# Kernel tuning notes

Measured on AMD Instinct MI355X. Metric: run time of the kernel, lower is better.

Reference implementation:

```python
import jax, jax.numpy as jnp
import numpy as np

PAD = 32  # integer padding from init_kwargs

def _conv1d_fft(x, weight, bias):
    # x: (B, Cin, L), weight: (Cout, Cin, K), bias: (Cout,)
    B, Cin, L = x.shape
    Cout, _, K = weight.shape
    p = PAD
    padded = (L + 2 * p + 31) & ~31          # round up to multiple of 32
    out_len = 2 * p + L - (K - 1)
    offset = (min(K, L) - 1) // 2 - p
    roll = -((K - 1) // 2) + offset
    # pad kernel to padded length then circularly roll (centers the kernel)
    k_pad = jnp.pad(weight, ((0, 0), (0, 0), (0, padded - K)))
    k_rolled = jnp.roll(k_pad, roll, axis=-1)
    x_fft = jnp.fft.rfft(x, n=padded, axis=-1)          # (B, Cin, F)
    k_fft = jnp.fft.rfft(k_rolled, axis=-1)             # (Cout, Cin, F)
    # multiply-reduce over in_channels == batched complex GEMM over freq bins
    b_fft = jnp.einsum('bif,oif->bof', x_fft, jnp.conj(k_fft))
    # bias enters only the DC bin, scaled by padded length (irfft normalization)
    b_fft = b_fft.at[..., 0].add(bias.astype(b_fft.dtype) * padded)
    b = jnp.fft.irfft(b_fft, n=padded, axis=-1)
    return b[..., :out_len]


def setup_inputs() -> dict:
    key = jax.random.key(0)
    k1, k2, k3 = jax.random.split(key, 3)
    B, Cin, Cout, L, K = 16, 128, 128, 4096, 129
    stdv = 1.0 / np.sqrt(Cin * K)
    x = jax.random.normal(k1, (B, Cin, L), dtype=jnp.float32)
    weight = jax.random.uniform(k2, (Cout, Cin, K), dtype=jnp.float32, minval=-stdv, maxval=stdv)
    bias = jax.random.uniform(k3, (Cout,), dtype=jnp.float32, minval=-stdv, maxval=stdv)
    return {"x": x, "weight": weight, "bias": bias}


def reference(x, weight, bias):
    return _conv1d_fft(x, weight, bias)
```

## Files before the change

### kernel.cpp

```cpp
#include <hip/hip_runtime.h>


typedef _Float16 f16;
typedef _Float16 f16x8 __attribute__((ext_vector_type(8)));
typedef float f32x4 __attribute__((ext_vector_type(4)));

#define NB   16
#define CI   128
#define CO   128
#define LIN  4096
#define KW   129
#define TOUT 4032
#define UPAD 4224
#define KCH  516
#define XT_BYTES ((size_t)NB * UPAD * CI * 2)

__device__ __forceinline__ void gld16(void* lds, const void* g) {
    __builtin_amdgcn_global_load_lds(
        (const __attribute__((address_space(1))) unsigned int*)g,
        (__attribute__((address_space(3))) unsigned int*)lds,
        16, 0, 0);
}

__global__ __launch_bounds__(256) void xt_prep(const float* __restrict__ x,
                                               f16* __restrict__ xt) {
    __shared__ float tile[128][33];
    const int b  = blockIdx.y;
    const int u0 = blockIdx.x * 32;
    const int l0 = u0 - 32;
    const int tid = threadIdx.x;
    const int col = tid & 31;
    const int cib = tid >> 5;
#pragma unroll
    for (int r = 0; r < 16; ++r) {
        int ci = cib + r * 8;
        int l  = l0 + col;
        float v = 0.f;
        if (l >= 0 && l < LIN) v = x[((size_t)b * CI + ci) * LIN + l];
        tile[ci][col] = v;
    }
    __syncthreads();
#pragma unroll
    for (int it = 0; it < 2; ++it) {
        int idx  = tid + it * 256;
        int ur   = idx >> 4;
        int slot = idx & 15;
        int c    = slot ^ ((u0 + ur) & 7);
        f16x8 v;
#pragma unroll
        for (int j = 0; j < 8; ++j) v[j] = (f16)tile[c * 8 + j][ur];
        *(f16x8*)(&xt[((size_t)b * UPAD + u0 + ur) * CI + slot * 8]) = v;
    }
}

__global__ __launch_bounds__(256) void wt_prep(const float* __restrict__ w,
                                               f16* __restrict__ wt) {
    __shared__ float tile[32][132];
    const int cic = blockIdx.x;
    const int co  = blockIdx.y;
    const int ci0 = cic * 32;
    const int tid = threadIdx.x;
    for (int it = 0; it < 17; ++it) {
        int idx = tid + it * 256;
        if (idx < 32 * 129) {
            int i = idx / 129;
            int m = idx - i * 129;
            tile[i][m] = w[(size_t)co * (CI * KW) + (size_t)(ci0 + i) * KW + m];
        }
    }
    __syncthreads();
    const int swz = (co >> 1) & 3;
    for (int it = 0; it < 3; ++it) {
        int idx = tid + it * 256;
        if (idx < 129 * 4) {
            int m = idx >> 2;
            int c = idx & 3;
            int kk = m * 4 + cic;
            int slot = c ^ swz;
            f16x8 v;
#pragma unroll
            for (int j = 0; j < 8; ++j) v[j] = (f16)tile[c * 8 + j][m];
            *(f16x8*)(&wt[((size_t)kk * 128 + co) * 32 + slot * 8]) = v;
        }
    }
}

__global__ __launch_bounds__(256, 3) void conv_main(
    const f16* __restrict__ xt, const f16* __restrict__ wt,
    const float* __restrict__ bias, float* __restrict__ out)
{
    extern __shared__ char smem[];
    const int tid  = threadIdx.x;
    const int lane = tid & 63;
    const int wid  = tid >> 6;
    const int l15  = lane & 15;
    const int l4   = lane >> 4;
    const int wco  = (wid >> 1) << 6;
    const int wtt  = (wid & 1) << 6;

    const int tt = blockIdx.x;
    const int b  = blockIdx.y;
    const int u0 = tt << 7;

    const char* xbase = (const char*)xt + ((size_t)b * UPAD + u0) * (CI * 2);
    const char* wbase = (const char*)wt;

    const int aslotx = (l4 ^ ((l15 >> 1) & 3)) << 4;
    int aoff[4];
#pragma unroll
    for (int ct = 0; ct < 4; ++ct)
        aoff[ct] = ((wco + ct * 16 + l15) << 6) + aslotx;

    int brow[4];
#pragma unroll
    for (int st = 0; st < 4; ++st)
        brow[st] = wtt + st * 16 + l15;

    f32x4 acc[4][4];
#pragma unroll
    for (int i = 0; i < 4; ++i)
#pragma unroll
        for (int j = 0; j < 4; ++j)
            acc[i][j] = (f32x4){0.f, 0.f, 0.f, 0.f};

    for (int p = 0; p < 2; ++p) {
#pragma unroll
        for (int i = 0; i < 8; ++i) {
            int off   = tid * 16 + i * 4096;
            int row   = off >> 7;
            int inrow = off & 127;
            gld16(smem + off, xbase + row * 256 + p * 128 + inrow);
        }
        {
            const char* wsrc = wbase + (size_t)(2 * p) * 8192;
            gld16(smem + 32768 + tid * 16, wsrc + tid * 16);
            gld16(smem + 32768 + 4096 + tid * 16, wsrc + 4096 + tid * 16);
        }
        __syncthreads();

#pragma unroll 2
        for (int s = 0; s < 258; ++s) {
            const int bufo = (s & 1) << 13;
            if (s + 1 < 258) {
                int sn    = s + 1;
                int chunk = ((sn >> 1) << 2) + 2 * p + (sn & 1);
                const char* wsrc = wbase + (size_t)chunk * 8192;
                int nbufo = 8192 - bufo;
                gld16(smem + 32768 + nbufo + tid * 16, wsrc + tid * 16);
                gld16(smem + 32768 + nbufo + 4096 + tid * 16, wsrc + 4096 + tid * 16);
            }
            const int m  = s >> 1;
            const int cl = ((s & 1) << 2) + l4;

            f16x8 af[4], bf[4];
#pragma unroll
            for (int ct = 0; ct < 4; ++ct)
                af[ct] = *(const f16x8*)(smem + 32768 + bufo + aoff[ct]);
#pragma unroll
            for (int st = 0; st < 4; ++st) {
                int row  = brow[st] + m;
                int slot = cl ^ (row & 7);
                bf[st] = *(const f16x8*)(smem + (row << 7) + (slot << 4));
            }
#pragma unroll
            for (int ct = 0; ct < 4; ++ct)
#pragma unroll
                for (int st = 0; st < 4; ++st)
                    acc[ct][st] = __builtin_amdgcn_mfma_f32_16x16x32_f16(
                        af[ct], bf[st], acc[ct][st], 0, 0, 0);
            __syncthreads();
        }
    }

#pragma unroll
    for (int ct = 0; ct < 4; ++ct) {
#pragma unroll
        for (int r = 0; r < 4; ++r) {
            int co = wco + ct * 16 + l4 * 4 + r;
            float bv = bias[co];
            float* orow = out + ((size_t)b * CO + co) * TOUT;
#pragma unroll
            for (int st = 0; st < 4; ++st) {
                int t = u0 + wtt + st * 16 + l15;
                if (t < TOUT) orow[t] = acc[ct][st][r] + bv;
            }
        }
    }
}

extern "C" void kernel_launch(void* const* d_in, const int* in_sizes, int n_in,
                              void* d_out, int out_size, void* d_ws, size_t ws_size,
                              hipStream_t stream) {
    const float* x    = (const float*)d_in[0];
    const float* w    = (const float*)d_in[1];
    const float* bias = (const float*)d_in[2];
    float* out = (float*)d_out;

    f16* xt = (f16*)d_ws;
    f16* wt = (f16*)((char*)d_ws + XT_BYTES);

    xt_prep<<<dim3(UPAD / 32, NB), 256, 0, stream>>>(x, xt);
    wt_prep<<<dim3(4, CO), 256, 0, stream>>>(w, wt);
    conv_main<<<dim3(32, NB), 256, 49152, stream>>>(xt, wt, bias, out);
}
```

Before: 329.5 us.

## Load weight fragments directly from global into registers, drop per-step LDS barrier

Weight tiles are no longer staged through a double-buffered LDS region. Each wave now loads its A fragments straight from global memory (L2/L1 cached) into registers, prefetched one step ahead. This removes the per-iteration __syncthreads and cuts LDS to 32 KB. The swizzle on the weight layout is dropped to match the new direct reads. In exchange, every wave issues redundant global loads whose latency must be hidden by the one-step register prefetch, and launch_bounds drops to 2 blocks per CU, which allows more registers per thread.

New measurement: 365.5 us. +10.9%, slower.

```diff
diff --git a/kernel.cpp b/kernel.cpp
--- a/kernel.cpp
+++ b/kernel.cpp
@@ -12,7 +12,6 @@
 #define KW   129
 #define TOUT 4032
 #define UPAD 4224
-#define KCH  516
 #define XT_BYTES ((size_t)NB * UPAD * CI * 2)
 
 __device__ __forceinline__ void gld16(void* lds, const void* g) {
@@ -69,23 +68,21 @@
         }
     }
     __syncthreads();
-    const int swz = (co >> 1) & 3;
     for (int it = 0; it < 3; ++it) {
         int idx = tid + it * 256;
         if (idx < 129 * 4) {
             int m = idx >> 2;
             int c = idx & 3;
             int kk = m * 4 + cic;
-            int slot = c ^ swz;
             f16x8 v;
 #pragma unroll
             for (int j = 0; j < 8; ++j) v[j] = (f16)tile[c * 8 + j][m];
-            *(f16x8*)(&wt[((size_t)kk * 128 + co) * 32 + slot * 8]) = v;
-        }
-    }
-}
-
-__global__ __launch_bounds__(256, 3) void conv_main(
+            *(f16x8*)(&wt[((size_t)kk * 128 + co) * 32 + c * 8]) = v;
+        }
+    }
+}
+
+__global__ __launch_bounds__(256, 2) void conv_main(
     const f16* __restrict__ xt, const f16* __restrict__ wt,
     const float* __restrict__ bias, float* __restrict__ out)
 {
@@ -105,11 +102,10 @@
     const char* xbase = (const char*)xt + ((size_t)b * UPAD + u0) * (CI * 2);
     const char* wbase = (const char*)wt;
 
-    const int aslotx = (l4 ^ ((l15 >> 1) & 3)) << 4;
-    int aoff[4];
+    int wrow_off[4];
 #pragma unroll
     for (int ct = 0; ct < 4; ++ct)
-        aoff[ct] = ((wco + ct * 16 + l15) << 6) + aslotx;
+        wrow_off[ct] = (wco + ct * 16 + l15) * 64 + l4 * 16;
 
     int brow[4];
 #pragma unroll
@@ -124,6 +120,7 @@
             acc[i][j] = (f32x4){0.f, 0.f, 0.f, 0.f};
 
     for (int p = 0; p < 2; ++p) {
+        if (p) __syncthreads();
 #pragma unroll
         for (int i = 0; i < 8; ++i) {
             int off   = tid * 16 + i * 4096;
@@ -131,31 +128,27 @@
             int inrow = off & 127;
             gld16(smem + off, xbase + row * 256 + p * 128 + inrow);
         }
-        {
-            const char* wsrc = wbase + (size_t)(2 * p) * 8192;
-            gld16(smem + 32768 + tid * 16, wsrc + tid * 16);
-            gld16(smem + 32768 + 4096 + tid * 16, wsrc + 4096 + tid * 16);
-        }
         __syncthreads();
+
+        const char* wp = wbase + p * (2 * 8192);
+
+        f16x8 af[4], an[4];
+#pragma unroll
+        for (int ct = 0; ct < 4; ++ct)
+            af[ct] = *(const f16x8*)(wp + wrow_off[ct]);
 
 #pragma unroll 2
         for (int s = 0; s < 258; ++s) {
-            const int bufo = (s & 1) << 13;
-            if (s + 1 < 258) {
-                int sn    = s + 1;
-                int chunk = ((sn >> 1) << 2) + 2 * p + (sn & 1);
-                const char* wsrc = wbase + (size_t)chunk * 8192;
-                int nbufo = 8192 - bufo;
-                gld16(smem + 32768 + nbufo + tid * 16, wsrc + tid * 16);
-                gld16(smem + 32768 + nbufo + 4096 + tid * 16, wsrc + 4096 + tid * 16);
-            }
+            const int sp = (s + 1 < 258) ? s + 1 : 257;
+            const int o  = (sp >> 1) * 32768 + (sp & 1) * 8192;
+#pragma unroll
+            for (int ct = 0; ct < 4; ++ct)
+                an[ct] = *(const f16x8*)(wp + o + wrow_off[ct]);
+
             const int m  = s >> 1;
             const int cl = ((s & 1) << 2) + l4;
 
-            f16x8 af[4], bf[4];
-#pragma unroll
-            for (int ct = 0; ct < 4; ++ct)
-                af[ct] = *(const f16x8*)(smem + 32768 + bufo + aoff[ct]);
+            f16x8 bf[4];
 #pragma unroll
             for (int st = 0; st < 4; ++st) {
                 int row  = brow[st] + m;
@@ -168,7 +161,9 @@
                 for (int st = 0; st < 4; ++st)
                     acc[ct][st] = __builtin_amdgcn_mfma_f32_16x16x32_f16(
                         af[ct], bf[st], acc[ct][st], 0, 0, 0);
-            __syncthreads();
+#pragma unroll
+            for (int ct = 0; ct < 4; ++ct)
+                af[ct] = an[ct];
         }
     }
 
@@ -201,5 +196,5 @@
 
     xt_prep<<<dim3(UPAD / 32, NB), 256, 0, stream>>>(x, xt);
     wt_prep<<<dim3(4, CO), 256, 0, stream>>>(w, wt);
-    conv_main<<<dim3(32, NB), 256, 49152, stream>>>(xt, wt, bias, out);
-}
+    conv_main<<<dim3(32, NB), 256, 32768, stream>>>(xt, wt, bias, out);
+}
```

## Triple-buffer weight tiles with one barrier per k-step and partial vmcnt waits

Applied to the files above, without the earlier changes.

The weight LDS buffering goes from two stages to three. Each k-step now issues the next prefetch, waits only for the older loads with vmcnt(2), then does a single barrier before the MFMAs, replacing the trailing __syncthreads that drained every outstanding load. The loop is manually unrolled by three to rotate the buffer indices, and launch bounds drop from 3 to 2 waves per SIMD to make room for the larger 56KB LDS footprint. The aim is to overlap global-to-LDS loads with compute, at the risk of lower occupancy.

Result: no change. 329.4 us (-0.0%).

```diff
diff --git a/kernel.cpp b/kernel.cpp
--- a/kernel.cpp
+++ b/kernel.cpp
@@ -12,8 +12,8 @@
 #define KW   129
 #define TOUT 4032
 #define UPAD 4224
-#define KCH  516
 #define XT_BYTES ((size_t)NB * UPAD * CI * 2)
+#define WLDS 32768
 
 __device__ __forceinline__ void gld16(void* lds, const void* g) {
     __builtin_amdgcn_global_load_lds(
@@ -85,7 +85,7 @@
     }
 }
 
-__global__ __launch_bounds__(256, 3) void conv_main(
+__global__ __launch_bounds__(256, 2) void conv_main(
     const f16* __restrict__ xt, const f16* __restrict__ wt,
     const float* __restrict__ bias, float* __restrict__ out)
 {
@@ -124,6 +124,9 @@
             acc[i][j] = (f32x4){0.f, 0.f, 0.f, 0.f};
 
     for (int p = 0; p < 2; ++p) {
+        const int pbase = 2 * p;
+
+        __builtin_amdgcn_s_barrier();
 #pragma unroll
         for (int i = 0; i < 8; ++i) {
             int off   = tid * 16 + i * 4096;
@@ -132,30 +135,33 @@
             gld16(smem + off, xbase + row * 256 + p * 128 + inrow);
         }
         {
-            const char* wsrc = wbase + (size_t)(2 * p) * 8192;
-            gld16(smem + 32768 + tid * 16, wsrc + tid * 16);
-            gld16(smem + 32768 + 4096 + tid * 16, wsrc + 4096 + tid * 16);
-        }
-        __syncthreads();
-
-#pragma unroll 2
-        for (int s = 0; s < 258; ++s) {
-            const int bufo = (s & 1) << 13;
-            if (s + 1 < 258) {
-                int sn    = s + 1;
-                int chunk = ((sn >> 1) << 2) + 2 * p + (sn & 1);
-                const char* wsrc = wbase + (size_t)chunk * 8192;
-                int nbufo = 8192 - bufo;
-                gld16(smem + 32768 + nbufo + tid * 16, wsrc + tid * 16);
-                gld16(smem + 32768 + nbufo + 4096 + tid * 16, wsrc + 4096 + tid * 16);
+            const char* wsrc = wbase + (size_t)pbase * 8192;
+            gld16(smem + WLDS + tid * 16,        wsrc + tid * 16);
+            gld16(smem + WLDS + 4096 + tid * 16, wsrc + 4096 + tid * 16);
+        }
+        asm volatile("s_waitcnt vmcnt(0)" ::: "memory");
+        __builtin_amdgcn_s_barrier();
+
+        auto kstep = [&](int s, int rb, int pb, bool pf) {
+            if (pf) {
+                const int sp = s + 1;
+                const int kk = (sp >> 1) * 4 + pbase + (sp & 1);
+                const char* wsrc = wbase + (size_t)kk * 8192;
+                gld16(smem + WLDS + pb * 8192 + tid * 16,        wsrc + tid * 16);
+                gld16(smem + WLDS + pb * 8192 + 4096 + tid * 16, wsrc + 4096 + tid * 16);
+                asm volatile("s_waitcnt vmcnt(2)" ::: "memory");
+            } else {
+                asm volatile("s_waitcnt vmcnt(0)" ::: "memory");
             }
+            __builtin_amdgcn_s_barrier();
+
             const int m  = s >> 1;
             const int cl = ((s & 1) << 2) + l4;
-
+            const char* wlds = smem + WLDS + rb * 8192;
             f16x8 af[4], bf[4];
 #pragma unroll
             for (int ct = 0; ct < 4; ++ct)
-                af[ct] = *(const f16x8*)(smem + 32768 + bufo + aoff[ct]);
+                af[ct] = *(const f16x8*)(wlds + aoff[ct]);
 #pragma unroll
             for (int st = 0; st < 4; ++st) {
                 int row  = brow[st] + m;
@@ -168,8 +174,17 @@
                 for (int st = 0; st < 4; ++st)
                     acc[ct][st] = __builtin_amdgcn_mfma_f32_16x16x32_f16(
                         af[ct], bf[st], acc[ct][st], 0, 0, 0);
-            __syncthreads();
-        }
+        };
+
+        for (int g = 0; g < 85; ++g) {
+            int s = g * 3;
+            kstep(s,     0, 1, true);
+            kstep(s + 1, 1, 2, true);
+            kstep(s + 2, 2, 0, true);
+        }
+        kstep(255, 0, 1, true);
+        kstep(256, 1, 2, true);
+        kstep(257, 2, 0, false);
     }
 
 #pragma unroll
@@ -201,5 +216,5 @@
 
     xt_prep<<<dim3(UPAD / 32, NB), 256, 0, stream>>>(x, xt);
     wt_prep<<<dim3(4, CO), 256, 0, stream>>>(w, wt);
-    conv_main<<<dim3(32, NB), 256, 49152, stream>>>(xt, wt, bias, out);
-}
+    conv_main<<<dim3(32, NB), 256, 57344, stream>>>(xt, wt, bias, out);
+}
```
